# Kernel tuning notes

Measured on AMD Instinct MI355X. Metric: run time of the kernel, lower is better.

Reference implementation:

```python
import jax, jax.numpy as jnp
import numpy as np
import math

D_MODEL = 1024
NUM_HEADS = 16
D_K = D_MODEL // NUM_HEADS
ROPE_THETA = 10000.0


def _rope(x, pos):
    # x: [b, h, s, d], pos: [s] int -> apply interleaved rotary embedding
    d = x.shape[-1]
    inv_freq = 1.0 / (ROPE_THETA ** (jnp.arange(0, d, 2, dtype=jnp.float32) / d))  # [d/2]
    angles = pos.astype(jnp.float32)[:, None] * inv_freq  # [s, d/2]
    cos = jnp.cos(angles)  # broadcast to [1,1,s,d/2]
    sin = jnp.sin(angles)
    x1 = x[..., 0::2]
    x2 = x[..., 1::2]
    o1 = x1 * cos - x2 * sin
    o2 = x1 * sin + x2 * cos
    return jnp.stack([o1, o2], axis=-1).reshape(x.shape)


def setup_inputs() -> dict:
    key = jax.random.key(0)
    kx, kq, kk, kv, ko = jax.random.split(key, 5)
    scale = 1.0 / math.sqrt(D_MODEL)
    x = jax.random.normal(kx, (2, 2048, D_MODEL), dtype=jnp.float32)
    token_positions = jnp.arange(2048, dtype=jnp.int32)
    Wq = jax.random.normal(kq, (D_MODEL, D_MODEL), dtype=jnp.float32) * scale
    Wk = jax.random.normal(kk, (D_MODEL, D_MODEL), dtype=jnp.float32) * scale
    Wv = jax.random.normal(kv, (D_MODEL, D_MODEL), dtype=jnp.float32) * scale
    Wo = jax.random.normal(ko, (D_MODEL, D_MODEL), dtype=jnp.float32) * scale
    return {"x": x, "token_positions": token_positions, "Wq": Wq, "Wk": Wk, "Wv": Wv, "Wo": Wo}


def reference(x, token_positions, Wq, Wk, Wv, Wo):
    b, s, _ = x.shape
    h, dk = NUM_HEADS, D_K
    # Linear stores weight as [out, in]; y = x @ W.T
    def proj(W):
        y = jnp.einsum('bsm,nm->bsn', x, W)
        return y.reshape(b, s, h, dk).transpose(0, 2, 1, 3)  # [b,h,s,dk]
    Q = _rope(proj(Wq), token_positions)
    K = _rope(proj(Wk), token_positions)
    V = proj(Wv)
    scores = jnp.einsum('bhqd,bhkd->bhqk', Q, K) / math.sqrt(dk)
    causal = jnp.arange(s)[:, None] >= jnp.arange(s)[None, :]  # [s,s]
    scores = jnp.where(causal, scores, -jnp.inf)
    weights = jax.nn.softmax(scores, axis=-1)
    attn = jnp.einsum('bhqk,bhkd->bhqd', weights, V)  # [b,h,s,dk]
    attn = attn.transpose(0, 2, 1, 3).reshape(b, s, h * dk)
    return jnp.einsum('bsn,mn->bsm', attn, Wo)
```

## Files before the change

### kernel.cpp

```cpp
#include <hip/hip_runtime.h>
#include <math.h>

#define SEQ   2048
#define BATCH 2
#define NH    16
#define DKD   64
#define DM    1024
#define MTOT  (BATCH*SEQ)

typedef short bf16x8 __attribute__((ext_vector_type(8)));
typedef float f32x4  __attribute__((ext_vector_type(4)));
typedef unsigned short u16x4 __attribute__((ext_vector_type(4)));

#define MFMA_B16(a,b,c) __builtin_amdgcn_mfma_f32_16x16x32_bf16((a),(b),(c),0,0,0)

__device__ __forceinline__ unsigned short f2bf(float f) {
    union { float f; unsigned int u; } v; v.f = f;
    unsigned int r = v.u + 0x7FFFu + ((v.u >> 16) & 1u);
    return (unsigned short)(r >> 16);
}
__device__ __forceinline__ float bf2f(unsigned short h) {
    union { unsigned int u; float f; } v; v.u = ((unsigned int)h) << 16;
    return v.f;
}
__device__ __forceinline__ void gload16(const void* g, void* l) {
    __builtin_amdgcn_global_load_lds(
        (const __attribute__((address_space(1))) unsigned int*)g,
        (__attribute__((address_space(3))) unsigned int*)l, 16, 0, 0);
}

__global__ __launch_bounds__(256)
void convert_all(const float* __restrict__ x,  const float* __restrict__ Wq,
                 const float* __restrict__ Wk, const float* __restrict__ Wv,
                 const float* __restrict__ Wo,
                 unsigned short* __restrict__ Xb, unsigned short* __restrict__ Wqkvb,
                 unsigned short* __restrict__ Wob)
{
    int i = blockIdx.x * 256 + threadIdx.x;
    const float* src;
    unsigned short* dst;
    size_t off;
    if (i < (1 << 20)) {
        src = x; dst = Xb; off = (size_t)i;
    } else {
        int j = i - (1 << 20);
        int wsel = j >> 18;
        off = (size_t)(j & ((1 << 18) - 1));
        src = (wsel == 0) ? Wq : (wsel == 1) ? Wk : (wsel == 2) ? Wv : Wo;
        dst = (wsel < 3) ? Wqkvb + (size_t)wsel * (1u << 20) : Wob;
    }
    float4 v = ((const float4*)src)[off];
    u16x4 o = { f2bf(v.x), f2bf(v.y), f2bf(v.z), f2bf(v.w) };
    *(u16x4*)&dst[off * 4] = o;
}

__global__ __launch_bounds__(256)
void rope_bf16(unsigned short* __restrict__ Qb, unsigned short* __restrict__ Kb,
               const int* __restrict__ pos)
{
    int g = blockIdx.x * 256 + threadIdx.x;
    int tsel = g >> 20;
    int i = g & ((1 << 20) - 1);
    unsigned short* base = tsel ? Kb : Qb;
    int d4 = i & 15;
    int s  = (i >> 4) & (SEQ - 1);
    float P = (float)pos[s];
    const float NEG_L2 = -0.41524101186092103f;
    int p0 = d4 * 2, p1 = p0 + 1;
    float a0 = P * exp2f((float)p0 * NEG_L2);
    float a1 = P * exp2f((float)p1 * NEG_L2);
    float s0, c0, s1, c1;
    sincosf(a0, &s0, &c0);
    sincosf(a1, &s1, &c1);

    u16x4 v = *(u16x4*)&base[(size_t)i * 4];
    float x0 = bf2f(v[0]), x1 = bf2f(v[1]), x2 = bf2f(v[2]), x3 = bf2f(v[3]);
    u16x4 o = { f2bf(x0 * c0 - x1 * s0), f2bf(x0 * s0 + x1 * c0),
                f2bf(x2 * c1 - x3 * s1), f2bf(x2 * s1 + x3 * c1) };
    *(u16x4*)&base[(size_t)i * 4] = o;
}

template<int MODE>
__global__ __launch_bounds__(256)
void gemm_mfma(const unsigned short* __restrict__ A, const unsigned short* __restrict__ B,
               unsigned short* __restrict__ Qb, unsigned short* __restrict__ Kb,
               unsigned short* __restrict__ VTb, float* __restrict__ Cf)
{
    const int t = threadIdx.x;
    const int w = t >> 6, l = t & 63, lid = l & 15, hi = (l >> 4) * 16;
    const int wm = w >> 1, wn = w & 1;
    const int m0 = blockIdx.y * 128, n0 = blockIdx.x * 128;

    __shared__ __align__(16) char At[2][8192];
    __shared__ __align__(16) char Bt[2][8192];

    f32x4 acc[4][4];
    const f32x4 z4 = {0.f, 0.f, 0.f, 0.f};
    #pragma unroll
    for (int i = 0; i < 4; ++i)
        #pragma unroll
        for (int j = 0; j < 4; ++j) acc[i][j] = z4;

    const char* Ab = (const char*)A;
    const char* Bb = (const char*)B;

    auto stage = [&](int buf, int kt) {
        const int kbyte = kt * 64;
        #pragma unroll
        for (int i = 0; i < 2; ++i) {
            int o   = i * 4096 + t * 16;
            int row = o >> 6, cb = o & 63;
            char* lbase_a = At[buf] + i * 4096 + (t >> 6) * 1024;
            char* lbase_b = Bt[buf] + i * 4096 + (t >> 6) * 1024;
            gload16(Ab + (size_t)(m0 + row) * 2048 + kbyte + cb, lbase_a);
            gload16(Bb + (size_t)(n0 + row) * 2048 + kbyte + cb, lbase_b);
        }
    };

    stage(0, 0);
    __syncthreads();

    const int NKT = DM / 32;
    for (int kt = 0; kt < NKT; ++kt) {
        const int cur = kt & 1;
        if (kt + 1 < NKT) stage(cur ^ 1, kt + 1);

        bf16x8 af[4], bfr[4];
        #pragma unroll
        for (int mf = 0; mf < 4; ++mf)
            af[mf] = *(const bf16x8*)(At[cur] + (wm * 64 + mf * 16 + lid) * 64 + hi);
        #pragma unroll
        for (int nf = 0; nf < 4; ++nf)
            bfr[nf] = *(const bf16x8*)(Bt[cur] + (wn * 64 + nf * 16 + lid) * 64 + hi);
        __builtin_amdgcn_s_setprio(1);
        #pragma unroll
        for (int mf = 0; mf < 4; ++mf)
            #pragma unroll
            for (int nf = 0; nf < 4; ++nf)
                acc[mf][nf] = MFMA_B16(af[mf], bfr[nf], acc[mf][nf]);
        __builtin_amdgcn_s_setprio(0);

        __syncthreads();
    }

    if (MODE == 1) {
        #pragma unroll
        for (int mf = 0; mf < 4; ++mf)
            #pragma unroll
            for (int nf = 0; nf < 4; ++nf) {
                int ncol = n0 + wn * 64 + nf * 16 + lid;
                #pragma unroll
                for (int jj = 0; jj < 4; ++jj) {
                    int mrow = m0 + wm * 64 + mf * 16 + (l >> 4) * 4 + jj;
                    Cf[(size_t)mrow * DM + ncol] = acc[mf][nf][jj];
                }
            }
    } else {
        const int z = n0 >> 10;
        const int nbase = n0 & 1023;
        #pragma unroll
        for (int mf = 0; mf < 4; ++mf)
            #pragma unroll
            for (int nf = 0; nf < 4; ++nf) {
                int ncol = nbase + wn * 64 + nf * 16 + lid;
                int h = ncol >> 6, d = ncol & 63;
                int mbase = m0 + wm * 64 + mf * 16 + (l >> 4) * 4;
                int b = mbase >> 11, s0v = mbase & 2047;
                if (z == 2) {
                    u16x4 pk = { f2bf(acc[mf][nf][0]), f2bf(acc[mf][nf][1]),
                                 f2bf(acc[mf][nf][2]), f2bf(acc[mf][nf][3]) };
                    *(u16x4*)&VTb[((size_t)(b * NH + h) * DKD + d) * SEQ + s0v] = pk;
                } else {
                    unsigned short* dst = (z == 0) ? Qb : Kb;
                    #pragma unroll
                    for (int jj = 0; jj < 4; ++jj)
                        dst[((size_t)(b * NH + h) * SEQ + (s0v + jj)) * DKD + d] =
                            f2bf(acc[mf][nf][jj]);
                }
            }
    }
}

__global__ __launch_bounds__(512)
void flash_mfma(const unsigned short* __restrict__ Qb, const unsigned short* __restrict__ Kb,
                const unsigned short* __restrict__ VTb, unsigned short* __restrict__ AOb)
{
    const int L  = blockIdx.y * 16 + blockIdx.x;
    const int g  = L >> 8, c = L & 255;
    const int j  = c & 15;
    const int bh = (g << 4) | (c >> 4);
    const int b = bh >> 4, h = bh & 15;
    const int qbA = g ? (30 - 2 * j) : (2 * j);
    const int qbB = qbA + 1;

    const int t = threadIdx.x;
    const int w8 = t >> 6, l = t & 63, lid = l & 15, hi = (l >> 4) * 16;
    const int h4 = l >> 4;
    const int tile = w8 >> 2, wq = w8 & 3;
    const int qbMy = tile ? qbB : qbA;
    const int ntMy = qbMy + 1;
    const int q0My = qbMy * 64;
    const int ntB  = qbB + 1;

    __shared__ __align__(16) char Kt[3][8192];
    __shared__ __align__(16) char Vt[3][8192];
    __shared__ __align__(16) char Pt[2][8192];

    const char* Kbh = (const char*)(Kb  + (size_t)bh * SEQ * DKD);
    const char* Vbh = (const char*)(VTb + (size_t)bh * SEQ * DKD);
    const char* Qbh = (const char*)(Qb  + (size_t)bh * SEQ * DKD);

    const f32x4 z4 = {0.f, 0.f, 0.f, 0.f};
    const int qrow = wq * 16 + lid;
    const float CLOG = 0.18033688011112042f;
    const float NMC  = -17.312340490667560f;

    bf16x8 onesv;
    #pragma unroll
    for (int i = 0; i < 8; ++i) onesv[i] = (short)0x3F80;

    bf16x8 qf[2];
    qf[0] = *(const bf16x8*)(Qbh + (size_t)(q0My + qrow) * 128 + 0  + hi);
    qf[1] = *(const bf16x8*)(Qbh + (size_t)(q0My + qrow) * 128 + 64 + hi);

    f32x4 o[4], o5;
    #pragma unroll
    for (int nf = 0; nf < 4; ++nf) o[nf] = z4;
    o5 = z4;

    auto stage = [&](int buf, int kt) {
        const int k0 = kt * 64;
        int o_  = t * 16;
        int row = o_ >> 7, cl = o_ & 127;
        int sw  = (row & 7) << 4;
        char* lK = Kt[buf] + w8 * 1024;
        char* lV = Vt[buf] + w8 * 1024;
        gload16(Kbh + (size_t)(k0 + row) * 128 + (cl ^ sw), lK);
        gload16(Vbh + (size_t)row * (SEQ * 2) + k0 * 2 + (cl ^ sw), lV);
    };

    stage(0, 0);
    stage(1, 1);

    for (int kt = 0; kt < ntB; ++kt) {
        const int cur = kt % 3;

        if (kt == ntB - 1) asm volatile("s_waitcnt vmcnt(0)" ::: "memory");
        else               asm volatile("s_waitcnt vmcnt(2)" ::: "memory");
        __builtin_amdgcn_s_barrier();
        if (kt + 2 < ntB) stage((kt + 2) % 3, kt + 2);

        if (kt < ntMy) {
            f32x4 sf[4];
            __builtin_amdgcn_s_setprio(1);
            #pragma unroll
            for (int nf = 0; nf < 4; ++nf) {
                f32x4 a = z4;
                #pragma unroll
                for (int ks = 0; ks < 2; ++ks) {
                    int r  = nf * 16 + lid;
                    int cb = ks * 64 + hi;
                    bf16x8 kfr = *(const bf16x8*)(Kt[cur] + r * 128 + (cb ^ ((r & 7) << 4)));
                    a = MFMA_B16(kfr, qf[ks], a);
                }
                sf[nf] = a;
            }
            __builtin_amdgcn_s_setprio(0);

            if (kt == qbMy) {
                const int qloc = wq * 16 + lid;
                #pragma unroll
                for (int nf = 0; nf < 4; ++nf) {
                    #pragma unroll
                    for (int jj = 0; jj < 4; ++jj) {
                        int keyloc = nf * 16 + h4 * 4 + jj;
                        if (keyloc > qloc) sf[nf][jj] = -1e30f;
                    }
                }
            }

            uint2 pk[4];
            #pragma unroll
            for (int nf = 0; nf < 4; ++nf) {
                float p0, p1, p2, p3;
                asm("v_exp_f32 %0, %1" : "=v"(p0) : "v"(fmaf(sf[nf][0], CLOG, NMC)));
                asm("v_exp_f32 %0, %1" : "=v"(p1) : "v"(fmaf(sf[nf][1], CLOG, NMC)));
                asm("v_exp_f32 %0, %1" : "=v"(p2) : "v"(fmaf(sf[nf][2], CLOG, NMC)));
                asm("v_exp_f32 %0, %1" : "=v"(p3) : "v"(fmaf(sf[nf][3], CLOG, NMC)));
                unsigned plo, phi;
                asm("v_cvt_pk_bf16_f32 %0, %1, %2" : "=v"(plo) : "v"(p0), "v"(p1));
                asm("v_cvt_pk_bf16_f32 %0, %1, %2" : "=v"(phi) : "v"(p2), "v"(p3));
                pk[nf].x = plo; pk[nf].y = phi;
            }

            {
                const int rowq = wq * 16 + lid;
                const int swz  = (lid & 7) << 4;
                char* base = Pt[tile] + rowq * 128;
                #pragma unroll
                for (int nf = 0; nf < 4; ++nf)
                    *(uint2*)(base + ((nf * 32 + 8 * h4) ^ swz)) = pk[nf];
            }

            #pragma unroll
            for (int ks = 0; ks < 2; ++ks) {
                int cb = ks * 64 + hi;
                int qr = wq * 16 + lid;
                bf16x8 pa = *(const bf16x8*)(Pt[tile] + qr * 128 + (cb ^ ((qr & 7) << 4)));
                __builtin_amdgcn_s_setprio(1);
                #pragma unroll
                for (int nf = 0; nf < 4; ++nf) {
                    int dr = nf * 16 + lid;
                    bf16x8 vb = *(const bf16x8*)(Vt[cur] + dr * 128 + (cb ^ ((dr & 7) << 4)));
                    o[nf] = MFMA_B16(pa, vb, o[nf]);
                }
                o5 = MFMA_B16(pa, onesv, o5);
                __builtin_amdgcn_s_setprio(0);
            }
        }
    }

    float inv[4];
    #pragma unroll
    for (int jj = 0; jj < 4; ++jj) inv[jj] = 1.0f / o5[jj];
    #pragma unroll
    for (int nf = 0; nf < 4; ++nf)
        #pragma unroll
        for (int jj = 0; jj < 4; ++jj) {
            int srow = q0My + wq * 16 + h4 * 4 + jj;
            int col  = h * 64 + nf * 16 + lid;
            AOb[((size_t)b * SEQ + srow) * DM + col] = f2bf(o[nf][jj] * inv[jj]);
        }
}

extern "C" void kernel_launch(void* const* d_in, const int* in_sizes, int n_in,
                              void* d_out, int out_size, void* d_ws, size_t ws_size,
                              hipStream_t stream)
{
    const float* x   = (const float*)d_in[0];
    const int*   pos = (const int*)  d_in[1];
    const float* Wq  = (const float*)d_in[2];
    const float* Wk  = (const float*)d_in[3];
    const float* Wv  = (const float*)d_in[4];
    const float* Wo  = (const float*)d_in[5];
    float* out = (float*)d_out;

    const size_t M1 = 1u << 20;
    unsigned short* ws  = (unsigned short*)d_ws;
    unsigned short* Xb    = ws;
    unsigned short* Wqkvb = ws + 4 * M1;
    unsigned short* Wob   = ws + 7 * M1;
    unsigned short* Qbf   = ws + 8 * M1;
    unsigned short* Kbf   = ws + 12 * M1;
    unsigned short* VTb   = ws + 16 * M1;
    unsigned short* AOb   = ws + 20 * M1;

    convert_all<<<8192, 256, 0, stream>>>(x, Wq, Wk, Wv, Wo, Xb, Wqkvb, Wob);

    gemm_mfma<0><<<dim3(24, 32), 256, 0, stream>>>(Xb, Wqkvb, Qbf, Kbf, VTb, nullptr);

    rope_bf16<<<8192, 256, 0, stream>>>(Qbf, Kbf, pos);

    flash_mfma<<<dim3(16, 32), 512, 0, stream>>>(Qbf, Kbf, VTb, AOb);

    gemm_mfma<1><<<dim3(8, 32), 256, 0, stream>>>(AOb, Wob, nullptr, nullptr, nullptr, out);
}
```

Measured before the change: 122.5 us.

## Triple-buffer GEMM with swizzled LDS and widen convert/rope vectors

The GEMM moves from a double-buffered to a triple-buffered LDS pipeline with two tiles in flight. It replaces the per-iteration __syncthreads with an explicit vmcnt wait plus s_barrier, and applies an XOR swizzle on LDS columns to reduce bank conflicts on fragment reads. The convert and rope kernels now handle 8 elements per thread instead of 4, halving the grid size. The main risks are the extra LDS use lowering occupancy and the correctness of the hand-tuned waitcnt and swizzle.

Result: faster. 119.5 us, median of 2 (-2.5%).

```diff
diff --git a/kernel.cpp b/kernel.cpp
--- a/kernel.cpp
+++ b/kernel.cpp
@@ -11,6 +11,7 @@
 typedef short bf16x8 __attribute__((ext_vector_type(8)));
 typedef float f32x4  __attribute__((ext_vector_type(4)));
 typedef unsigned short u16x4 __attribute__((ext_vector_type(4)));
+typedef unsigned short u16x8 __attribute__((ext_vector_type(8)));
 
 #define MFMA_B16(a,b,c) __builtin_amdgcn_mfma_f32_16x16x32_bf16((a),(b),(c),0,0,0)
 
@@ -40,44 +41,48 @@
     const float* src;
     unsigned short* dst;
     size_t off;
-    if (i < (1 << 20)) {
+    if (i < (1 << 19)) {
         src = x; dst = Xb; off = (size_t)i;
     } else {
-        int j = i - (1 << 20);
-        int wsel = j >> 18;
-        off = (size_t)(j & ((1 << 18) - 1));
+        int j = i - (1 << 19);
+        int wsel = j >> 17;
+        off = (size_t)(j & ((1 << 17) - 1));
         src = (wsel == 0) ? Wq : (wsel == 1) ? Wk : (wsel == 2) ? Wv : Wo;
         dst = (wsel < 3) ? Wqkvb + (size_t)wsel * (1u << 20) : Wob;
     }
-    float4 v = ((const float4*)src)[off];
-    u16x4 o = { f2bf(v.x), f2bf(v.y), f2bf(v.z), f2bf(v.w) };
-    *(u16x4*)&dst[off * 4] = o;
+    float4 v0 = ((const float4*)src)[off * 2];
+    float4 v1 = ((const float4*)src)[off * 2 + 1];
+    u16x8 o = { f2bf(v0.x), f2bf(v0.y), f2bf(v0.z), f2bf(v0.w),
+                f2bf(v1.x), f2bf(v1.y), f2bf(v1.z), f2bf(v1.w) };
+    *(u16x8*)&dst[off * 8] = o;
 }
 
 __global__ __launch_bounds__(256)
 void rope_bf16(unsigned short* __restrict__ Qb, unsigned short* __restrict__ Kb,
                const int* __restrict__ pos)
 {
-    int g = blockIdx.x * 256 + threadIdx.x;
-    int tsel = g >> 20;
-    int i = g & ((1 << 20) - 1);
+    int idx = blockIdx.x * 256 + threadIdx.x;
+    int tsel = idx >> 19;
+    int i = idx & ((1 << 19) - 1);
     unsigned short* base = tsel ? Kb : Qb;
-    int d4 = i & 15;
-    int s  = (i >> 4) & (SEQ - 1);
+    int d8 = i & 7;
+    int s  = (i >> 3) & (SEQ - 1);
     float P = (float)pos[s];
     const float NEG_L2 = -0.41524101186092103f;
-    int p0 = d4 * 2, p1 = p0 + 1;
-    float a0 = P * exp2f((float)p0 * NEG_L2);
-    float a1 = P * exp2f((float)p1 * NEG_L2);
-    float s0, c0, s1, c1;
-    sincosf(a0, &s0, &c0);
-    sincosf(a1, &s1, &c1);
-
-    u16x4 v = *(u16x4*)&base[(size_t)i * 4];
-    float x0 = bf2f(v[0]), x1 = bf2f(v[1]), x2 = bf2f(v[2]), x3 = bf2f(v[3]);
-    u16x4 o = { f2bf(x0 * c0 - x1 * s0), f2bf(x0 * s0 + x1 * c0),
-                f2bf(x2 * c1 - x3 * s1), f2bf(x2 * s1 + x3 * c1) };
-    *(u16x4*)&base[(size_t)i * 4] = o;
+
+    u16x8 v = *(u16x8*)&base[(size_t)i * 8];
+    u16x8 o;
+    #pragma unroll
+    for (int k = 0; k < 4; ++k) {
+        int pi = d8 * 4 + k;
+        float ang = P * exp2f((float)pi * NEG_L2);
+        float sn, cs;
+        sincosf(ang, &sn, &cs);
+        float e0 = bf2f(v[2*k]), e1 = bf2f(v[2*k + 1]);
+        o[2*k]     = f2bf(e0 * cs - e1 * sn);
+        o[2*k + 1] = f2bf(e0 * sn + e1 * cs);
+    }
+    *(u16x8*)&base[(size_t)i * 8] = o;
 }
 
 template<int MODE>
@@ -91,8 +96,8 @@
     const int wm = w >> 1, wn = w & 1;
     const int m0 = blockIdx.y * 128, n0 = blockIdx.x * 128;
 
-    __shared__ __align__(16) char At[2][8192];
-    __shared__ __align__(16) char Bt[2][8192];
+    __shared__ __align__(16) char At[3][8192];
+    __shared__ __align__(16) char Bt[3][8192];
 
     f32x4 acc[4][4];
     const f32x4 z4 = {0.f, 0.f, 0.f, 0.f};
@@ -110,28 +115,36 @@
         for (int i = 0; i < 2; ++i) {
             int o   = i * 4096 + t * 16;
             int row = o >> 6, cb = o & 63;
+            int sw  = ((row >> 1) & 3) << 4;
             char* lbase_a = At[buf] + i * 4096 + (t >> 6) * 1024;
             char* lbase_b = Bt[buf] + i * 4096 + (t >> 6) * 1024;
-            gload16(Ab + (size_t)(m0 + row) * 2048 + kbyte + cb, lbase_a);
-            gload16(Bb + (size_t)(n0 + row) * 2048 + kbyte + cb, lbase_b);
+            gload16(Ab + (size_t)(m0 + row) * 2048 + kbyte + (cb ^ sw), lbase_a);
+            gload16(Bb + (size_t)(n0 + row) * 2048 + kbyte + (cb ^ sw), lbase_b);
         }
     };
 
+    const int NKT = DM / 32;
     stage(0, 0);
-    __syncthreads();
-
-    const int NKT = DM / 32;
+    stage(1, 1);
+
     for (int kt = 0; kt < NKT; ++kt) {
-        const int cur = kt & 1;
-        if (kt + 1 < NKT) stage(cur ^ 1, kt + 1);
+        const int cur = kt % 3;
+        if (kt == NKT - 1) asm volatile("s_waitcnt vmcnt(0)" ::: "memory");
+        else               asm volatile("s_waitcnt vmcnt(4)" ::: "memory");
+        __builtin_amdgcn_s_barrier();
+        if (kt + 2 < NKT) stage((kt + 2) % 3, kt + 2);
 
         bf16x8 af[4], bfr[4];
         #pragma unroll
-        for (int mf = 0; mf < 4; ++mf)
-            af[mf] = *(const bf16x8*)(At[cur] + (wm * 64 + mf * 16 + lid) * 64 + hi);
-        #pragma unroll
-        for (int nf = 0; nf < 4; ++nf)
-            bfr[nf] = *(const bf16x8*)(Bt[cur] + (wn * 64 + nf * 16 + lid) * 64 + hi);
+        for (int mf = 0; mf < 4; ++mf) {
+            int ar = wm * 64 + mf * 16 + lid;
+            af[mf] = *(const bf16x8*)(At[cur] + ar * 64 + (hi ^ (((ar >> 1) & 3) << 4)));
+        }
+        #pragma unroll
+        for (int nf = 0; nf < 4; ++nf) {
+            int br = wn * 64 + nf * 16 + lid;
+            bfr[nf] = *(const bf16x8*)(Bt[cur] + br * 64 + (hi ^ (((br >> 1) & 3) << 4)));
+        }
         __builtin_amdgcn_s_setprio(1);
         #pragma unroll
         for (int mf = 0; mf < 4; ++mf)
@@ -139,8 +152,6 @@
             for (int nf = 0; nf < 4; ++nf)
                 acc[mf][nf] = MFMA_B16(af[mf], bfr[nf], acc[mf][nf]);
         __builtin_amdgcn_s_setprio(0);
-
-        __syncthreads();
     }
 
     if (MODE == 1) {
@@ -355,11 +366,11 @@
     unsigned short* VTb   = ws + 16 * M1;
     unsigned short* AOb   = ws + 20 * M1;
 
-    convert_all<<<8192, 256, 0, stream>>>(x, Wq, Wk, Wv, Wo, Xb, Wqkvb, Wob);
+    convert_all<<<4096, 256, 0, stream>>>(x, Wq, Wk, Wv, Wo, Xb, Wqkvb, Wob);
 
     gemm_mfma<0><<<dim3(24, 32), 256, 0, stream>>>(Xb, Wqkvb, Qbf, Kbf, VTb, nullptr);
 
-    rope_bf16<<<8192, 256, 0, stream>>>(Qbf, Kbf, pos);
+    rope_bf16<<<4096, 256, 0, stream>>>(Qbf, Kbf, pos);
 
     flash_mfma<<<dim3(16, 32), 512, 0, stream>>>(Qbf, Kbf, VTb, AOb);
 
```
